# Performance work log

Hardware: AMD Instinct MI355X
Metric: run time of the kernel (lower is better)

The kernel has to match this reference:

```python
import jax, jax.numpy as jnp
import numpy as np

N_VOX = 200000
Z, Y, X = 41, 256, 256


def _build_rulebook(N, seed=0):
    """Build submanifold 3x3x3 rulebook: nbr[i,k] = voxel index of neighbor k of voxel i, or -1."""
    rng = np.random.default_rng(seed)
    keys = np.unique(rng.integers(0, Z * Y * X, size=int(N * 1.3)))
    assert keys.shape[0] >= N
    keys = keys[:N]  # sorted unique linearized coords
    z = keys // (Y * X)
    rem = keys % (Y * X)
    y = rem // X
    x = rem % X
    nbr = np.full((N, 27), -1, np.int32)
    k = 0
    for dz in (-1, 0, 1):
        for dy in (-1, 0, 1):
            for dx in (-1, 0, 1):
                nz, ny, nx = z + dz, y + dy, x + dx
                valid = (nz >= 0) & (nz < Z) & (ny >= 0) & (ny < Y) & (nx >= 0) & (nx < X)
                nkey = (nz * Y + ny) * X + nx
                pos = np.searchsorted(keys, nkey)
                pos_c = np.minimum(pos, N - 1)
                found = valid & (keys[pos_c] == nkey)
                nbr[:, k] = np.where(found, pos_c, -1)
                k += 1
    return nbr


def setup_inputs() -> dict:
    key = jax.random.key(0)
    ks = jax.random.split(key, 8)
    nbr = jnp.asarray(_build_rulebook(N_VOX))
    return {
        "voxel_features": jax.random.normal(ks[0], (N_VOX, 4), jnp.float32),
        "nbr_idx": nbr,
        "W0": jax.random.normal(ks[1], (27, 4, 16), jnp.float32) * 0.05,
        "s0": jnp.ones((16,), jnp.float32),
        "b0": jnp.zeros((16,), jnp.float32),
        "W1": jax.random.normal(ks[2], (27, 16, 16), jnp.float32) * 0.05,
        "s1": jnp.ones((16,), jnp.float32),
        "b1": jnp.zeros((16,), jnp.float32),
        "W2": jax.random.normal(ks[3], (27, 16, 16), jnp.float32) * 0.05,
        "s2": jnp.ones((16,), jnp.float32),
        "b2": jnp.zeros((16,), jnp.float32),
        "W_lin": jax.random.normal(ks[4], (16, 3), jnp.float32) * 0.05,
        "b_lin": jnp.zeros((3,), jnp.float32),
    }


def _subm_conv(feats, W, nbr, mask):
    # feats: [N, Cin], W: [27, Cin, Cout], nbr: [N, 27] (rulebook), mask: [N, 27, 1]
    g = jnp.take(feats, jnp.maximum(nbr, 0), axis=0) * mask  # [N, 27, Cin] gather (memory-bound)
    return jnp.einsum("nkc,kcd->nd", g, W)  # scatter-free dense contraction


def reference(voxel_features, nbr_idx, W0, s0, b0, W1, s1, b1, W2, s2, b2, W_lin, b_lin):
    mask = (nbr_idx >= 0)[..., None].astype(voxel_features.dtype)
    # conv_input: SubMConv3d(4,16,3) + BN(folded to scale/shift) + ReLU
    x = jax.nn.relu(_subm_conv(voxel_features, W0, nbr_idx, mask) * s0 + b0)
    # SparseBasicBlock(16,16, indice_key='subm1'): conv-bn-relu-conv-bn + residual + relu
    idn = x
    h = jax.nn.relu(_subm_conv(x, W1, nbr_idx, mask) * s1 + b1)
    h = _subm_conv(h, W2, nbr_idx, mask) * s2 + b2
    x = jax.nn.relu(h + idn)
    # mos_seg_layer: Linear(16, mos_class)
    return x @ W_lin + b_lin
```

## Files before the change

kernel.cpp:

```cpp
#include <hip/hip_runtime.h>

#define NVOX 200000
#define TILE 256
#define WINROWS 256
#define NWIN 5
#define ETG (NWIN * WINROWS)
#define NTILES ((NVOX + TILE - 1) / TILE)
#define NBINS (NWIN * 27)

__device__ __forceinline__ void fma16x16(const float4* __restrict__ wrow,
                                         float4 f0, float4 f1, float4 f2, float4 f3,
                                         float acc[16]) {
    const float g[16] = {f0.x, f0.y, f0.z, f0.w, f1.x, f1.y, f1.z, f1.w,
                         f2.x, f2.y, f2.z, f2.w, f3.x, f3.y, f3.z, f3.w};
    #pragma unroll
    for (int cc = 0; cc < 16; ++cc) {
        float gc = g[cc];
        float4 w0 = wrow[cc * 4 + 0];
        float4 w1 = wrow[cc * 4 + 1];
        float4 w2 = wrow[cc * 4 + 2];
        float4 w3 = wrow[cc * 4 + 3];
        acc[0]  += gc * w0.x; acc[1]  += gc * w0.y; acc[2]  += gc * w0.z; acc[3]  += gc * w0.w;
        acc[4]  += gc * w1.x; acc[5]  += gc * w1.y; acc[6]  += gc * w1.z; acc[7]  += gc * w1.w;
        acc[8]  += gc * w2.x; acc[9]  += gc * w2.y; acc[10] += gc * w2.z; acc[11] += gc * w2.w;
        acc[12] += gc * w3.x; acc[13] += gc * w3.y; acc[14] += gc * w3.z; acc[15] += gc * w3.w;
    }
}

__global__ __launch_bounds__(256) void k1_compact_conv0(
    const float* __restrict__ feats,
    const int* __restrict__ nbr,
    const float* __restrict__ W,
    const float* __restrict__ s, const float* __restrict__ b,
    int* __restrict__ gEnt,
    unsigned short* __restrict__ gVm,
    int* __restrict__ rowstartG,
    int* __restrict__ wbaseG,
    float* __restrict__ x) {
    __shared__ int   lnbr[TILE * 27];
    __shared__ __align__(16) float Wl[27 * 68];
    __shared__ int   bhist[NBINS];
    __shared__ int   bbase[NBINS];
    __shared__ int   rs[TILE];
    __shared__ int   eloc[ETG];
    __shared__ unsigned short evm[ETG];
    int t = threadIdx.x;
    int tile = blockIdx.x;
    int base = tile * TILE;
    for (int i = t; i < 27 * 64; i += 256)
        Wl[(i >> 6) * 68 + (i & 63)] = W[i];
    for (int i = t; i < NBINS; i += 256) bhist[i] = 0;
    int nv = NVOX - base; if (nv > TILE) nv = TILE;
    const int* gsrc = nbr + base * 27;
    for (int i = t; i < nv * 27; i += 256)
        lnbr[i] = gsrc[i];
    __syncthreads();

    int c = 0;
    int* row = lnbr + t * 27;
    if (t < nv) {
        #pragma unroll
        for (int k = 0; k < 27; ++k) {
            int idx = row[k];
            if (idx >= 0) { row[c] = (idx << 5) | k; ++c; }
        }
    }
    rs[t] = c;
    __syncthreads();
    #pragma unroll
    for (int off = 1; off < TILE; off <<= 1) {
        int v = rs[t];
        if (t >= off) v += rs[t - off];
        __syncthreads();
        rs[t] = v;
        __syncthreads();
    }
    int excl = rs[t] - c;
    int total = rs[TILE - 1];
    int tot = total < ETG ? total : ETG;
    rowstartG[tile * (TILE + 1) + t] = excl < tot ? excl : tot;
    if (t == TILE - 1) rowstartG[tile * (TILE + 1) + TILE] = tot;

    for (int j = 0; j < c; ++j) {
        int vm = excl + j;
        if (vm < ETG) {
            int k = row[j] & 31;
            atomicAdd(&bhist[(vm >> 8) * 27 + k], 1);
        }
    }
    __syncthreads();
    if (t == 0) {
        int a = 0;
        for (int i = 0; i < NBINS; ++i) { bbase[i] = a; a += bhist[i]; }
        for (int w = 0; w < NWIN; ++w)
            wbaseG[tile * (NWIN + 1) + w] = bbase[w * 27];
        wbaseG[tile * (NWIN + 1) + NWIN] = a;
    }
    __syncthreads();
    for (int i = t; i < NBINS; i += 256) bhist[i] = 0;
    __syncthreads();
    for (int j = 0; j < c; ++j) {
        int vm = excl + j;
        if (vm < ETG) {
            int e = row[j];
            int bin = (vm >> 8) * 27 + (e & 31);
            int pos = bbase[bin] + atomicAdd(&bhist[bin], 1);
            eloc[pos] = e;
            evm[pos] = (unsigned short)vm;
        }
    }
    __syncthreads();
    for (int i = t; i < tot; i += 256) {
        gEnt[tile * ETG + i] = eloc[i];
        gVm[tile * ETG + i]  = evm[i];
    }

    if (t >= nv) return;
    float acc[16];
    #pragma unroll
    for (int d = 0; d < 16; ++d) acc[d] = 0.f;
    int e = row[0];
    float4 f = *(const float4*)(feats + (e >> 5) * 4);
    int j = 0;
    while (true) {
        bool more = (++j < c);
        int en = e; float4 fn = f;
        if (more) {
            en = row[j];
            fn = *(const float4*)(feats + (en >> 5) * 4);
        }
        {
            const float4* wrow = (const float4*)(Wl + (e & 31) * 68);
            float g[4] = {f.x, f.y, f.z, f.w};
            #pragma unroll
            for (int cc = 0; cc < 4; ++cc) {
                float gc = g[cc];
                float4 w0 = wrow[cc * 4 + 0];
                float4 w1 = wrow[cc * 4 + 1];
                float4 w2 = wrow[cc * 4 + 2];
                float4 w3 = wrow[cc * 4 + 3];
                acc[0]  += gc * w0.x; acc[1]  += gc * w0.y; acc[2]  += gc * w0.z; acc[3]  += gc * w0.w;
                acc[4]  += gc * w1.x; acc[5]  += gc * w1.y; acc[6]  += gc * w1.z; acc[7]  += gc * w1.w;
                acc[8]  += gc * w2.x; acc[9]  += gc * w2.y; acc[10] += gc * w2.z; acc[11] += gc * w2.w;
                acc[12] += gc * w3.x; acc[13] += gc * w3.y; acc[14] += gc * w3.z; acc[15] += gc * w3.w;
            }
        }
        if (!more) break;
        e = en; f = fn;
    }
    int n = base + t;
    float4* o = (float4*)(x + n * 16);
    #pragma unroll
    for (int q = 0; q < 4; ++q) {
        float4 r;
        float v0 = acc[q * 4 + 0] * s[q * 4 + 0] + b[q * 4 + 0];
        float v1 = acc[q * 4 + 1] * s[q * 4 + 1] + b[q * 4 + 1];
        float v2 = acc[q * 4 + 2] * s[q * 4 + 2] + b[q * 4 + 2];
        float v3 = acc[q * 4 + 3] * s[q * 4 + 3] + b[q * 4 + 3];
        r.x = v0 > 0.f ? v0 : 0.f;
        r.y = v1 > 0.f ? v1 : 0.f;
        r.z = v2 > 0.f ? v2 : 0.f;
        r.w = v3 > 0.f ? v3 : 0.f;
        o[q] = r;
    }
}

__device__ __forceinline__ void conv16_windowed(const float* __restrict__ fin,
                                                const int* __restrict__ gE,
                                                const unsigned short* __restrict__ gV,
                                                const int* __restrict__ wb,
                                                const float* __restrict__ Wl,
                                                float* __restrict__ partial,
                                                int rstart, int rend, int t,
                                                float acc[16]) {
    #pragma unroll
    for (int d = 0; d < 16; ++d) acc[d] = 0.f;
    for (int w = 0; w < NWIN; ++w) {
        int lo = w * WINROWS;
        int ebeg = wb[w], eend = wb[w + 1];
        for (int i = ebeg + t; i < eend; i += 256) {
            int e = gE[i];
            int vm = gV[i];
            const float4* fp = (const float4*)(fin + (e >> 5) * 16);
            float4 f0 = fp[0], f1 = fp[1], f2 = fp[2], f3 = fp[3];
            float pa[16];
            #pragma unroll
            for (int d = 0; d < 16; ++d) pa[d] = 0.f;
            fma16x16((const float4*)(Wl + (e & 31) * 260), f0, f1, f2, f3, pa);
            float4* pr = (float4*)(partial + (vm - lo) * 20);
            #pragma unroll
            for (int q = 0; q < 4; ++q) {
                float4 r;
                r.x = pa[q * 4 + 0]; r.y = pa[q * 4 + 1];
                r.z = pa[q * 4 + 2]; r.w = pa[q * 4 + 3];
                pr[q] = r;
            }
        }
        __syncthreads();
        int a  = rstart > lo ? rstart : lo;
        int bd = rend < lo + WINROWS ? rend : lo + WINROWS;
        for (int r = a; r < bd; ++r) {
            const float4* pr = (const float4*)(partial + (r - lo) * 20);
            #pragma unroll
            for (int q = 0; q < 4; ++q) {
                float4 v = pr[q];
                acc[q * 4 + 0] += v.x; acc[q * 4 + 1] += v.y;
                acc[q * 4 + 2] += v.z; acc[q * 4 + 3] += v.w;
            }
        }
        __syncthreads();
    }
}

__global__ __launch_bounds__(256, 3) void k2_conv1(
    const float* __restrict__ fin,
    const int* __restrict__ gEnt, const unsigned short* __restrict__ gVm,
    const int* __restrict__ rowstartG, const int* __restrict__ wbaseG,
    const float* __restrict__ W,
    const float* __restrict__ s, const float* __restrict__ b,
    float* __restrict__ out) {
    __shared__ __align__(16) float Wl[27 * 260];
    __shared__ __align__(16) float partial[WINROWS * 20];
    __shared__ int rs[TILE + 1];
    __shared__ int wb[NWIN + 1];
    int t = threadIdx.x;
    int tile = blockIdx.x;
    for (int i = t; i < 27 * 256; i += 256)
        Wl[(i >> 8) * 260 + (i & 255)] = W[i];
    rs[t] = rowstartG[tile * (TILE + 1) + t];
    if (t == 0) rs[TILE] = rowstartG[tile * (TILE + 1) + TILE];
    if (t < NWIN + 1) wb[t] = wbaseG[tile * (NWIN + 1) + t];
    __syncthreads();
    int rstart = rs[t];
    int rend = rs[t + 1];
    float acc[16];
    conv16_windowed(fin, gEnt + tile * ETG, gVm + tile * ETG, wb, Wl, partial,
                    rstart, rend, t, acc);
    int n = tile * TILE + t;
    if (n >= NVOX) return;
    float4* o = (float4*)(out + n * 16);
    #pragma unroll
    for (int q = 0; q < 4; ++q) {
        float4 r;
        float v0 = acc[q * 4 + 0] * s[q * 4 + 0] + b[q * 4 + 0];
        float v1 = acc[q * 4 + 1] * s[q * 4 + 1] + b[q * 4 + 1];
        float v2 = acc[q * 4 + 2] * s[q * 4 + 2] + b[q * 4 + 2];
        float v3 = acc[q * 4 + 3] * s[q * 4 + 3] + b[q * 4 + 3];
        r.x = v0 > 0.f ? v0 : 0.f;
        r.y = v1 > 0.f ? v1 : 0.f;
        r.z = v2 > 0.f ? v2 : 0.f;
        r.w = v3 > 0.f ? v3 : 0.f;
        o[q] = r;
    }
}

__global__ __launch_bounds__(256, 3) void k3_conv2_final(
    const float* __restrict__ fin,
    const int* __restrict__ gEnt, const unsigned short* __restrict__ gVm,
    const int* __restrict__ rowstartG, const int* __restrict__ wbaseG,
    const float* __restrict__ W,
    const float* __restrict__ s, const float* __restrict__ b,
    const float* __restrict__ idn,
    const float* __restrict__ Wlin,
    const float* __restrict__ blin,
    float* __restrict__ out) {
    __shared__ __align__(16) float Wl[27 * 260];
    __shared__ __align__(16) float partial[WINROWS * 20];
    __shared__ int rs[TILE + 1];
    __shared__ int wb[NWIN + 1];
    int t = threadIdx.x;
    int tile = blockIdx.x;
    for (int i = t; i < 27 * 256; i += 256)
        Wl[(i >> 8) * 260 + (i & 255)] = W[i];
    rs[t] = rowstartG[tile * (TILE + 1) + t];
    if (t == 0) rs[TILE] = rowstartG[tile * (TILE + 1) + TILE];
    if (t < NWIN + 1) wb[t] = wbaseG[tile * (NWIN + 1) + t];
    __syncthreads();
    int rstart = rs[t];
    int rend = rs[t + 1];
    float acc[16];
    conv16_windowed(fin, gEnt + tile * ETG, gVm + tile * ETG, wb, Wl, partial,
                    rstart, rend, t, acc);
    int n = tile * TILE + t;
    if (n >= NVOX) return;
    const float4* ip = (const float4*)(idn + n * 16);
    float4 i0 = ip[0], i1 = ip[1], i2 = ip[2], i3 = ip[3];
    float id[16] = {i0.x, i0.y, i0.z, i0.w, i1.x, i1.y, i1.z, i1.w,
                    i2.x, i2.y, i2.z, i2.w, i3.x, i3.y, i3.z, i3.w};
    float o0 = blin[0], o1 = blin[1], o2 = blin[2];
    #pragma unroll
    for (int d = 0; d < 16; ++d) {
        float v = acc[d] * s[d] + b[d] + id[d];
        v = v > 0.f ? v : 0.f;
        o0 += v * Wlin[d * 3 + 0];
        o1 += v * Wlin[d * 3 + 1];
        o2 += v * Wlin[d * 3 + 2];
    }
    out[n * 3 + 0] = o0;
    out[n * 3 + 1] = o1;
    out[n * 3 + 2] = o2;
}

extern "C" void kernel_launch(void* const* d_in, const int* in_sizes, int n_in,
                              void* d_out, int out_size, void* d_ws, size_t ws_size,
                              hipStream_t stream) {
    const float* feats = (const float*)d_in[0];
    const int*   nbr   = (const int*)d_in[1];
    const float* W0    = (const float*)d_in[2];
    const float* s0    = (const float*)d_in[3];
    const float* b0    = (const float*)d_in[4];
    const float* W1    = (const float*)d_in[5];
    const float* s1    = (const float*)d_in[6];
    const float* b1    = (const float*)d_in[7];
    const float* W2    = (const float*)d_in[8];
    const float* s2    = (const float*)d_in[9];
    const float* b2    = (const float*)d_in[10];
    const float* Wlin  = (const float*)d_in[11];
    const float* blin  = (const float*)d_in[12];
    float* out = (float*)d_out;

    char* ws = (char*)d_ws;
    int*            gEnt      = (int*)(ws);
    unsigned short* gVm       = (unsigned short*)(ws + 4003840);
    int*            rowstartG = (int*)(ws + 6005760);
    int*            wbaseG    = (int*)(ws + 6809664);
    float*          x         = (float*)(ws + 6828448);
    float*          h         = (float*)(ws + 19628448);

    k1_compact_conv0<<<NTILES, TILE, 0, stream>>>(feats, nbr, W0, s0, b0,
                                                  gEnt, gVm, rowstartG, wbaseG, x);
    k2_conv1<<<NTILES, TILE, 0, stream>>>(x, gEnt, gVm, rowstartG, wbaseG, W1, s1, b1, h);
    k3_conv2_final<<<NTILES, TILE, 0, stream>>>(h, gEnt, gVm, rowstartG, wbaseG, W2, s2, b2,
                                                x, Wlin, blin, out);
}
```

Baseline: 81.83 us.

## Halve window size and software-prefetch next window's gathered features

The conv windows shrink from 256 to 128 rows and their count doubles, so each thread handles at most one entry per window. While the current window is computed, each thread loads the next window's rulebook entry and its 16-channel feature gather into registers. The thread-to-entry mapping rotates between windows so the active half moves across waves. The smaller partial buffer in LDS allows the launch bound to rise from 3 to 4 blocks per CU. In exchange there are twice as many barrier-separated windows, only half the threads are active per window, and register pressure rises from holding the prefetched data.

```diff
diff --git a/kernel.cpp b/kernel.cpp
--- a/kernel.cpp
+++ b/kernel.cpp
@@ -2,8 +2,9 @@
 
 #define NVOX 200000
 #define TILE 256
-#define WINROWS 256
-#define NWIN 5
+#define WINROWS 128
+#define WSHIFT 7
+#define NWIN 10
 #define ETG (NWIN * WINROWS)
 #define NTILES ((NVOX + TILE - 1) / TILE)
 #define NBINS (NWIN * 27)
@@ -85,7 +86,7 @@
         int vm = excl + j;
         if (vm < ETG) {
             int k = row[j] & 31;
-            atomicAdd(&bhist[(vm >> 8) * 27 + k], 1);
+            atomicAdd(&bhist[(vm >> WSHIFT) * 27 + k], 1);
         }
     }
     __syncthreads();
@@ -103,7 +104,7 @@
         int vm = excl + j;
         if (vm < ETG) {
             int e = row[j];
-            int bin = (vm >> 8) * 27 + (e & 31);
+            int bin = (vm >> WSHIFT) * 27 + (e & 31);
             int pos = bbase[bin] + atomicAdd(&bhist[bin], 1);
             eloc[pos] = e;
             evm[pos] = (unsigned short)vm;
@@ -175,14 +176,36 @@
                                                 float acc[16]) {
     #pragma unroll
     for (int d = 0; d < 16; ++d) acc[d] = 0.f;
+    bool act = false;
+    int e = 0, vm = 0;
+    float4 f0, f1, f2, f3;
+    {
+        int i0 = wb[0] + t;
+        act = (t < WINROWS) && (i0 < wb[1]);
+        if (act) {
+            e = gE[i0];
+            vm = gV[i0];
+            const float4* fp = (const float4*)(fin + (e >> 5) * 16);
+            f0 = fp[0]; f1 = fp[1]; f2 = fp[2]; f3 = fp[3];
+        }
+    }
     for (int w = 0; w < NWIN; ++w) {
         int lo = w * WINROWS;
-        int ebeg = wb[w], eend = wb[w + 1];
-        for (int i = ebeg + t; i < eend; i += 256) {
-            int e = gE[i];
-            int vm = gV[i];
-            const float4* fp = (const float4*)(fin + (e >> 5) * 16);
-            float4 f0 = fp[0], f1 = fp[1], f2 = fp[2], f3 = fp[3];
+        bool act2 = false;
+        int e2 = 0, vm2 = 0;
+        float4 g0, g1, g2, g3;
+        if (w + 1 < NWIN) {
+            int rt = (t + (((w + 1) & 3) << 6)) & 255;
+            int i2 = wb[w + 1] + rt;
+            act2 = (rt < WINROWS) && (i2 < wb[w + 2]);
+            if (act2) {
+                e2 = gE[i2];
+                vm2 = gV[i2];
+                const float4* fq = (const float4*)(fin + (e2 >> 5) * 16);
+                g0 = fq[0]; g1 = fq[1]; g2 = fq[2]; g3 = fq[3];
+            }
+        }
+        if (act) {
             float pa[16];
             #pragma unroll
             for (int d = 0; d < 16; ++d) pa[d] = 0.f;
@@ -209,10 +232,12 @@
             }
         }
         __syncthreads();
-    }
-}
-
-__global__ __launch_bounds__(256, 3) void k2_conv1(
+        act = act2; e = e2; vm = vm2;
+        f0 = g0; f1 = g1; f2 = g2; f3 = g3;
+    }
+}
+
+__global__ __launch_bounds__(256, 4) void k2_conv1(
     const float* __restrict__ fin,
     const int* __restrict__ gEnt, const unsigned short* __restrict__ gVm,
     const int* __restrict__ rowstartG, const int* __restrict__ wbaseG,
@@ -254,7 +279,7 @@
     }
 }
 
-__global__ __launch_bounds__(256, 3) void k3_conv2_final(
+__global__ __launch_bounds__(256, 4) void k3_conv2_final(
     const float* __restrict__ fin,
     const int* __restrict__ gEnt, const unsigned short* __restrict__ gVm,
     const int* __restrict__ rowstartG, const int* __restrict__ wbaseG,
@@ -324,8 +349,8 @@
     unsigned short* gVm       = (unsigned short*)(ws + 4003840);
     int*            rowstartG = (int*)(ws + 6005760);
     int*            wbaseG    = (int*)(ws + 6809664);
-    float*          x         = (float*)(ws + 6828448);
-    float*          h         = (float*)(ws + 19628448);
+    float*          x         = (float*)(ws + 6844096);
+    float*          h         = (float*)(ws + 19644096);
 
     k1_compact_conv0<<<NTILES, TILE, 0, stream>>>(feats, nbr, W0, s0, b0,
                                                   gEnt, gVm, rowstartG, wbaseG, x);
```

Result: slower. 89.65 us (+9.6%).
